# Kernel optimization log

Measured on AMD Instinct MI355X. Metric: run time of the kernel, lower is better.

The kernel has to match this reference:

```python
import jax, jax.numpy as jnp
import numpy as np

C, H, V, K, B, T = 1024, 256, 10000, 32, 8, 256
K1K = 2 * K + 1


def setup_inputs() -> dict:
    key = jax.random.key(0)
    ks = jax.random.split(key, 12)
    s = 0.05
    n = lambda k, shp: jax.random.normal(k, shp, dtype=jnp.float32) * s
    z = lambda shp: jnp.zeros(shp, dtype=jnp.float32)
    return {
        'text': jax.random.randint(ks[0], (B, T), 0, V, dtype=jnp.int32),
        'start_emb': n(ks[1], (H,)),
        'start_lin_W': n(ks[2], (H, H)), 'start_lin_b': z((H,)),
        'start_res_W1': n(ks[3], (2, H, H)), 'start_res_b1': z((2, H)),
        'start_res_W2': n(ks[4], (2, H, H)), 'start_res_b2': z((2, H)),
        'state_emb': n(ks[5], (C, H)),
        'next_state_emb': n(ks[6], (C, H)),
        'preterminal_emb': n(ks[7], (C, H)),
        'term_res_W1': n(ks[8], (2, H, H)), 'term_res_b1': z((2, H)),
        'term_res_W2': n(ks[9], (2, H, H)), 'term_res_b2': z((2, H)),
        'terminal_emb': n(ks[10], (V, H)),
        'col_banded_transition': n(ks[11], (C, K1K)),
    }


def _res(x, W1, b1, W2, b2):
    # ResLayer: x + ReLU(Linear(ReLU(Linear(x))))
    h = jax.nn.relu(x @ W1.T + b1)
    h = jax.nn.relu(h @ W2.T + b2)
    return x + h


def _band_to_dense(band):
    # BandedMatrix(band[None], K, K, fill=0).to_dense(): dense[i, i+d] = band[i, d+K] for |d|<=K
    offs = jnp.arange(-K, K + 1)                  # (K1K,)
    rows = jnp.arange(C)
    cols = rows[:, None] + offs[None, :]          # (C, K1K)
    valid = (cols >= 0) & (cols < C)
    vals = jnp.where(valid, band, 0.0)
    return jnp.zeros((C, C), band.dtype).at[rows[:, None], jnp.clip(cols, 0, C - 1)].add(vals)


def reference(text, start_emb, start_lin_W, start_lin_b,
              start_res_W1, start_res_b1, start_res_W2, start_res_b2,
              state_emb, next_state_emb, preterminal_emb,
              term_res_W1, term_res_b1, term_res_W2, term_res_b2,
              terminal_emb, col_banded_transition):
    # start(): MLP(start_emb) @ next_state_emb.T (tie_start), log_softmax -> (C,)
    fx = start_emb @ start_lin_W.T + start_lin_b
    for i in range(2):
        fx = _res(fx, start_res_W1[i], start_res_b1[i], start_res_W2[i], start_res_b2[i])
    start = jax.nn.log_softmax(fx @ next_state_emb.T)

    # transition(): dense logits + banded logits (band_method='product'), row log_softmax -> (C, C)
    logits = state_emb @ next_state_emb.T
    trans = jax.nn.log_softmax(logits + _band_to_dense(col_banded_transition), axis=-1)

    # emission(): terminal_mlp(preterminal_emb) @ terminal_emb.T, log_softmax -> (C, V)
    ft = preterminal_emb
    for i in range(2):
        ft = _res(ft, term_res_W1[i], term_res_b1[i], term_res_W2[i], term_res_b2[i])
    emit_T = jax.nn.log_softmax(ft @ terminal_emb.T, axis=-1).T  # (V, C)

    # HMM forward algorithm over time (log semiring)
    alpha = start[None, :] + emit_T[text[:, 0]]  # (B, C)

    def step(alpha, toks):
        # alpha_next[b, j] = logsumexp_i(alpha[b, i] + trans[i, j]) + emit[j, tok_b]
        a = jax.nn.logsumexp(alpha[:, :, None] + trans[None], axis=1) + emit_T[toks]
        return a, None

    alpha, _ = jax.lax.scan(step, alpha, text[:, 1:].T)
    return jax.nn.logsumexp(alpha, axis=-1)  # (B,) log-evidence
```

## Files before the change

### kernel.cpp

```cpp
#include <hip/hip_runtime.h>

constexpr int C = 1024, H = 256, V = 10000, K = 32, B = 8, T = 256, K1K = 65;
constexpr int DB = 32;
constexpr int GSCAN = B * DB;
constexpr float LV = 9.210340371976184f;
constexpr unsigned SENT = 0x80000000u;

#define DEV static __device__ __forceinline__

typedef float f4 __attribute__((ext_vector_type(4)));

DEV void gstore(float* p, float v) {
  __hip_atomic_store((unsigned*)p, __float_as_uint(v), __ATOMIC_RELAXED, __HIP_MEMORY_SCOPE_AGENT);
}
DEV float gload(const float* p) {
  return __uint_as_float(__hip_atomic_load((unsigned*)p, __ATOMIC_RELAXED, __HIP_MEMORY_SCOPE_AGENT));
}

__global__ void __launch_bounds__(256) k_pre(
    const float* __restrict__ semb, const float* __restrict__ linW, const float* __restrict__ linb,
    const float* __restrict__ srW1, const float* __restrict__ srb1,
    const float* __restrict__ srW2, const float* __restrict__ srb2,
    const float* __restrict__ nse, const float* __restrict__ se,
    const float* __restrict__ pre, const float* __restrict__ trW1, const float* __restrict__ trb1,
    const float* __restrict__ trW2, const float* __restrict__ trb2,
    const float* __restrict__ band,
    float* __restrict__ pay, float* __restrict__ startv,
    float* __restrict__ ft, float* __restrict__ PT) {
  __shared__ float smem[10504];
  const int bid = blockIdx.x, tid = threadIdx.x;

  if (bid < 16) {
    unsigned* p = (unsigned*)pay;
    #pragma unroll
    for (int k = 0; k < 8; ++k) p[bid * 2048 + k * 256 + tid] = SENT;
    return;
  }

  if (bid == 16) {
    float* sa = smem;
    float* fx = smem + 256;
    float* hh = smem + 512;
    float* sl = smem + 768;
    float* red = smem + 1792;
    sa[tid] = semb[tid];
    __syncthreads();
    float acc = linb[tid];
    for (int h = 0; h < H; ++h) acc += sa[h] * linW[tid * H + h];
    fx[tid] = acc;
    __syncthreads();
    for (int l = 0; l < 2; ++l) {
      float a1 = srb1[l * H + tid];
      const float* w1 = srW1 + (size_t)l * H * H + (size_t)tid * H;
      for (int h = 0; h < H; ++h) a1 += fx[h] * w1[h];
      hh[tid] = fmaxf(a1, 0.f);
      __syncthreads();
      float a2 = srb2[l * H + tid];
      const float* w2 = srW2 + (size_t)l * H * H + (size_t)tid * H;
      for (int h = 0; h < H; ++h) a2 += hh[h] * w2[h];
      __syncthreads();
      fx[tid] += fmaxf(a2, 0.f);
      __syncthreads();
    }
    for (int q = 0; q < 4; ++q) {
      int c = q * 256 + tid;
      const float* nr = nse + (size_t)c * H;
      float s = 0.f;
      for (int h = 0; h < H; ++h) s += fx[h] * nr[h];
      sl[c] = s;
    }
    __syncthreads();
    float s = 0.f;
    for (int q = 0; q < 4; ++q) s += __expf(sl[q * 256 + tid]);
    red[tid] = s; __syncthreads();
    for (int off = 128; off > 0; off >>= 1) { if (tid < off) red[tid] += red[tid + off]; __syncthreads(); }
    float lse = __logf(red[0]);
    for (int q = 0; q < 4; ++q) { int c = q * 256 + tid; startv[c] = sl[c] - lse; }
    return;
  }

  if (bid < 81) {
    float* x = smem;
    float* hh = smem + 4096;
    int r0 = (bid - 17) * 16;
    for (int r = 0; r < 16; ++r) x[r * 256 + tid] = pre[(size_t)(r0 + r) * H + tid];
    __syncthreads();
    for (int l = 0; l < 2; ++l) {
      {
        const f4* w = (const f4*)(trW1 + (size_t)l * H * H + (size_t)tid * H);
        float a[16];
        #pragma unroll
        for (int r = 0; r < 16; ++r) a[r] = 0.f;
        for (int h4 = 0; h4 < H / 4; ++h4) {
          f4 wv = w[h4];
          #pragma unroll
          for (int r = 0; r < 16; ++r) {
            f4 xv = *(const f4*)&x[r * 256 + h4 * 4];
            a[r] += wv.x * xv.x + wv.y * xv.y + wv.z * xv.z + wv.w * xv.w;
          }
        }
        float bb = trb1[l * H + tid];
        #pragma unroll
        for (int r = 0; r < 16; ++r) hh[r * 256 + tid] = fmaxf(a[r] + bb, 0.f);
      }
      __syncthreads();
      {
        const f4* w = (const f4*)(trW2 + (size_t)l * H * H + (size_t)tid * H);
        float a[16];
        #pragma unroll
        for (int r = 0; r < 16; ++r) a[r] = 0.f;
        for (int h4 = 0; h4 < H / 4; ++h4) {
          f4 wv = w[h4];
          #pragma unroll
          for (int r = 0; r < 16; ++r) {
            f4 xv = *(const f4*)&hh[r * 256 + h4 * 4];
            a[r] += wv.x * xv.x + wv.y * xv.y + wv.z * xv.z + wv.w * xv.w;
          }
        }
        float bb = trb2[l * H + tid];
        #pragma unroll
        for (int r = 0; r < 16; ++r) x[r * 256 + tid] += fmaxf(a[r] + bb, 0.f);
      }
      __syncthreads();
    }
    for (int r = 0; r < 16; ++r) ft[(size_t)(r0 + r) * H + tid] = x[r * 256 + tid];
    return;
  }

  {
    float* sv = smem;
    float* sl = smem + 2048;
    float* pr = smem + 10240;
    float* iv = smem + 10496;
    int i0 = (bid - 81) * 8;
    for (int r = 0; r < 8; ++r) sv[r * 256 + tid] = se[(size_t)(i0 + r) * H + tid];
    __syncthreads();
    for (int jq = 0; jq < 4; ++jq) {
      int j = jq * 256 + tid;
      const f4* nr = (const f4*)(nse + (size_t)j * H);
      float a[8];
      #pragma unroll
      for (int r = 0; r < 8; ++r) a[r] = 0.f;
      for (int h4 = 0; h4 < H / 4; ++h4) {
        f4 nv = nr[h4];
        #pragma unroll
        for (int r = 0; r < 8; ++r) {
          f4 s4 = *(const f4*)&sv[r * 256 + h4 * 4];
          a[r] += nv.x * s4.x + nv.y * s4.y + nv.z * s4.z + nv.w * s4.w;
        }
      }
      #pragma unroll
      for (int r = 0; r < 8; ++r) sl[r * 1024 + j] = a[r];
    }
    __syncthreads();
    if (tid < K1K) {
      #pragma unroll
      for (int r = 0; r < 8; ++r) {
        int col = i0 + r + tid - K;
        if (col >= 0 && col < C) sl[r * 1024 + col] += band[(size_t)(i0 + r) * K1K + tid];
      }
    }
    __syncthreads();
    {
      int row = tid >> 5, lane32 = tid & 31;
      float s = 0.f;
      for (int k = 0; k < 32; ++k) {
        int idx = row * 1024 + lane32 + k * 32;
        float e = __expf(sl[idx]);
        sl[idx] = e;
        s += e;
      }
      pr[tid] = s;
    }
    __syncthreads();
    if (tid < 8) {
      float s = 0.f;
      for (int k = 0; k < 32; ++k) s += pr[tid * 32 + k];
      iv[tid] = 1.f / s;
    }
    __syncthreads();
    for (int jq = 0; jq < 4; ++jq) {
      int j = jq * 256 + tid;
      f4 o0, o1;
      o0.x = sl[0 * 1024 + j] * iv[0]; o0.y = sl[1 * 1024 + j] * iv[1];
      o0.z = sl[2 * 1024 + j] * iv[2]; o0.w = sl[3 * 1024 + j] * iv[3];
      o1.x = sl[4 * 1024 + j] * iv[4]; o1.y = sl[5 * 1024 + j] * iv[5];
      o1.z = sl[6 * 1024 + j] * iv[6]; o1.w = sl[7 * 1024 + j] * iv[7];
      f4* dst = (f4*)(PT + (size_t)j * C + i0);
      dst[0] = o0; dst[1] = o1;
    }
  }
}

__global__ void __launch_bounds__(256) k_denom_part(
    const float* __restrict__ ft, const float* __restrict__ term, float* __restrict__ dpart) {
  constexpr int TJ = 16, VC = V / 8;
  __shared__ float shs[TJ * 4];
  int tid = threadIdx.x, lane = tid & 63, w = tid >> 6;
  int jg = blockIdx.x >> 3, vc = blockIdx.x & 7;
  const f4* fb = (const f4*)(ft + (size_t)jg * TJ * H);
  float rs[TJ];
  #pragma unroll
  for (int r = 0; r < TJ; ++r) rs[r] = 0.f;
  int v0 = vc * VC;
  {
    const f4* t0 = (const f4*)(term + (size_t)(v0 + tid) * H);
    const f4* t1 = t0 + 256 * (H / 4);
    const f4* t2 = t1 + 256 * (H / 4);
    const f4* t3 = t2 + 256 * (H / 4);
    float a0[TJ], a1[TJ], a2[TJ], a3[TJ];
    #pragma unroll
    for (int r = 0; r < TJ; ++r) { a0[r] = 0.f; a1[r] = 0.f; a2[r] = 0.f; a3[r] = 0.f; }
    for (int h4 = 0; h4 < H / 4; ++h4) {
      f4 w0 = t0[h4], w1 = t1[h4], w2 = t2[h4], w3 = t3[h4];
      #pragma unroll
      for (int r = 0; r < TJ; ++r) {
        f4 f = fb[r * (H / 4) + h4];
        a0[r] += f.x * w0.x + f.y * w0.y + f.z * w0.z + f.w * w0.w;
        a1[r] += f.x * w1.x + f.y * w1.y + f.z * w1.z + f.w * w1.w;
        a2[r] += f.x * w2.x + f.y * w2.y + f.z * w2.z + f.w * w2.w;
        a3[r] += f.x * w3.x + f.y * w3.y + f.z * w3.z + f.w * w3.w;
      }
    }
    #pragma unroll
    for (int r = 0; r < TJ; ++r)
      rs[r] += __expf(a0[r]) + __expf(a1[r]) + __expf(a2[r]) + __expf(a3[r]);
  }
  if (tid < VC - 1024) {
    const f4* tt = (const f4*)(term + (size_t)(v0 + 1024 + tid) * H);
    float at[TJ];
    #pragma unroll
    for (int r = 0; r < TJ; ++r) at[r] = 0.f;
    for (int h4 = 0; h4 < H / 4; ++h4) {
      f4 wt = tt[h4];
      #pragma unroll
      for (int r = 0; r < TJ; ++r) {
        f4 f = fb[r * (H / 4) + h4];
        at[r] += f.x * wt.x + f.y * wt.y + f.z * wt.z + f.w * wt.w;
      }
    }
    #pragma unroll
    for (int r = 0; r < TJ; ++r) rs[r] += __expf(at[r]);
  }
  #pragma unroll
  for (int r = 0; r < TJ; ++r) {
    float s = rs[r];
    #pragma unroll
    for (int off = 32; off > 0; off >>= 1) s += __shfl_xor(s, off);
    if (lane == 0) shs[r * 4 + w] = s;
  }
  __syncthreads();
  if (tid < TJ) {
    float s = shs[tid * 4] + shs[tid * 4 + 1] + shs[tid * 4 + 2] + shs[tid * 4 + 3];
    dpart[(jg * TJ + tid) * 8 + vc] = s;
  }
}

__global__ void __launch_bounds__(256) k_eemit(
    const int* __restrict__ text, const float* __restrict__ ft,
    const float* __restrict__ dpart, const float* __restrict__ term,
    float* __restrict__ eem) {
  __shared__ float tk[32 * 256];
  __shared__ int ids[32];
  const int tid = threadIdx.x, bid = blockIdx.x;
  const int n0 = (bid >> 1) * 32, jh = bid & 1;
  if (tid < 32) {
    int n = n0 + tid;
    ids[tid] = text[(n & 7) * T + (n >> 3)];
  }
  __syncthreads();
  for (int r = 0; r < 32; ++r) tk[r * 256 + tid] = term[(size_t)ids[r] * H + tid];
  __syncthreads();
  for (int q = 0; q < 2; ++q) {
    int j = jh * 512 + q * 256 + tid;
    const f4* fr = (const f4*)(ft + (size_t)j * H);
    float acc[32];
    #pragma unroll
    for (int r = 0; r < 32; ++r) acc[r] = 0.f;
    for (int h4 = 0; h4 < H / 4; ++h4) {
      f4 fv = fr[h4];
      #pragma unroll
      for (int r = 0; r < 32; ++r) {
        f4 tv = *(const f4*)&tk[r * 256 + h4 * 4];
        acc[r] += fv.x * tv.x + fv.y * tv.y + fv.z * tv.z + fv.w * tv.w;
      }
    }
    f4 d0 = *(const f4*)&dpart[j * 8];
    f4 d1 = *(const f4*)&dpart[j * 8 + 4];
    float dj = __logf(d0.x + d0.y + d0.z + d0.w + d1.x + d1.y + d1.z + d1.w);
    #pragma unroll
    for (int r = 0; r < 32; ++r)
      eem[(size_t)(n0 + r) * C + j] = __expf(acc[r] - dj + LV);
  }
}

#define PLOADA(k, ofs) \
  asm volatile("global_load_dwordx4 %0, %1, off offset:" #ofs : "=v"(p##k) : "v"(pb));
#define PDOT(k) { f4 x = *(const f4*)&us[ubo + (k) * 4]; facc += p##k * x; }

__global__ void __launch_bounds__(256, 1) k_scan(
    const float* __restrict__ PT, const float* __restrict__ eem,
    const float* __restrict__ startv, float* __restrict__ pay,
    float* __restrict__ umax, float* __restrict__ out) {
  __shared__ __align__(16) float us[8 * 132];
  __shared__ __align__(16) float wv[32];
  __shared__ float fred[256];
  const int tid = threadIdx.x, bid = blockIdx.x;
  const int b = bid & 7, blk = bid >> 3;
  const int jloc = tid >> 3, s = tid & 7;
  const int myj = blk * 32 + jloc;
  const bool owner = (s == 0);

  const float* pb = PT + (size_t)myj * C + s * 128;
  f4 p0, p1, p2, p3, p4, p5, p6, p7, p8, p9, p10, p11, p12, p13, p14, p15;
  f4 p16, p17, p18, p19, p20, p21, p22, p23, p24, p25, p26, p27, p28, p29, p30, p31;
  PLOADA(0, 0)    PLOADA(1, 16)   PLOADA(2, 32)   PLOADA(3, 48)
  PLOADA(4, 64)   PLOADA(5, 80)   PLOADA(6, 96)   PLOADA(7, 112)
  PLOADA(8, 128)  PLOADA(9, 144)  PLOADA(10, 160) PLOADA(11, 176)
  PLOADA(12, 192) PLOADA(13, 208) PLOADA(14, 224) PLOADA(15, 240)
  PLOADA(16, 256) PLOADA(17, 272) PLOADA(18, 288) PLOADA(19, 304)
  PLOADA(20, 320) PLOADA(21, 336) PLOADA(22, 352) PLOADA(23, 368)
  PLOADA(24, 384) PLOADA(25, 400) PLOADA(26, 416) PLOADA(27, 432)
  PLOADA(28, 448) PLOADA(29, 464) PLOADA(30, 480) PLOADA(31, 496)

  float Sacc = 0.f;

  if (owner) {
    float u0 = __expf(startv[myj]) * eem[(size_t)b * C + myj];
    gstore(&pay[(size_t)b * C + myj], u0);
  }
  float em = owner ? eem[((size_t)B + b) * C + myj] : 0.f;

  const int pi = tid * 4;
  const int ph = (pi >> 7) * 132 + (pi & 127);
  const int ubo = s * 132;

  for (int t = 1; t < T; ++t) {
    {
      const float* src = pay + (size_t)((t - 1) & 3) * (B * C) + (size_t)b * C + pi;
      f4 r;
      for (;;) {
        asm volatile("global_load_dwordx4 %0, %1, off sc0 sc1\n\ts_waitcnt vmcnt(0)"
                     : "=v"(r) : "v"(src) : "memory");
        unsigned bits = __float_as_uint(r.x) | __float_as_uint(r.y) |
                        __float_as_uint(r.z) | __float_as_uint(r.w);
        if (!(bits & 0x80000000u)) break;
        __builtin_amdgcn_s_sleep(1);
      }
      *(f4*)&us[ph] = r;
    }
    __syncthreads();

    float em_next = em;
    if (owner && t + 1 < T) em_next = eem[((size_t)(t + 1) * B + b) * C + myj];

    float imt = 1.f;
    if (owner && (t & 7) == 1 && t > 1) {
      float m = gload(&umax[((t - 1) >> 3) * 8 + b]);
      imt = 1.f / m;
      Sacc += __logf(m);
    }

    f4 facc = {0.f, 0.f, 0.f, 0.f};
    PDOT(0) PDOT(1) PDOT(2) PDOT(3) PDOT(4) PDOT(5) PDOT(6) PDOT(7)
    PDOT(8) PDOT(9) PDOT(10) PDOT(11) PDOT(12) PDOT(13) PDOT(14) PDOT(15)
    PDOT(16) PDOT(17) PDOT(18) PDOT(19) PDOT(20) PDOT(21) PDOT(22) PDOT(23)
    PDOT(24) PDOT(25) PDOT(26) PDOT(27) PDOT(28) PDOT(29) PDOT(30) PDOT(31)
    float acc = facc.x + facc.y + facc.z + facc.w;
    acc += __shfl_xor(acc, 1);
    acc += __shfl_xor(acc, 2);
    acc += __shfl_xor(acc, 4);

    if (owner) wv[jloc] = acc * imt * em;
    __syncthreads();

    if (blk == 0 && (t & 7) == 0) {
      if (tid == 0) {
        float m = wv[0];
        #pragma unroll
        for (int j2 = 1; j2 < 32; ++j2) m = fmaxf(m, wv[j2]);
        gstore(&umax[(t >> 3) * 8 + b], m);
        asm volatile("s_waitcnt vmcnt(0)" ::: "memory");
      }
      __syncthreads();
    }

    if (tid < 8) {
      f4 pv4 = *(const f4*)&wv[tid * 4];
      float* dst = pay + (size_t)(t & 3) * (B * C) + (size_t)b * C + blk * 32 + tid * 4;
      asm volatile("global_store_dwordx4 %0, %1, off sc0 sc1" :: "v"(dst), "v"(pv4) : "memory");
    }

    if (tid < 8) {
      float* dst = pay + (size_t)((t + 2) & 3) * (B * C) + (size_t)b * C + blk * 32 + tid * 4;
      f4 sn;
      sn.x = sn.y = sn.z = sn.w = __uint_as_float(SENT);
      asm volatile("global_store_dwordx4 %0, %1, off sc0 sc1" :: "v"(dst), "v"(sn) : "memory");
    }
    em = em_next;
  }

  if (blk == 0) {
    {
      const float* src = pay + (size_t)((T - 1) & 3) * (B * C) + (size_t)b * C + pi;
      f4 r;
      for (;;) {
        asm volatile("global_load_dwordx4 %0, %1, off sc0 sc1\n\ts_waitcnt vmcnt(0)"
                     : "=v"(r) : "v"(src) : "memory");
        unsigned bits = __float_as_uint(r.x) | __float_as_uint(r.y) |
                        __float_as_uint(r.z) | __float_as_uint(r.w);
        if (!(bits & 0x80000000u)) break;
        __builtin_amdgcn_s_sleep(1);
      }
      fred[tid] = r.x + r.y + r.z + r.w;
    }
    __syncthreads();
    for (int off = 128; off > 0; off >>= 1) {
      if (tid < off) fred[tid] += fred[tid + off];
      __syncthreads();
    }
    if (tid == 0) out[b] = -(float)T * LV + Sacc + __logf(fred[0]);
  }
}

extern "C" void kernel_launch(void* const* d_in, const int* in_sizes, int n_in,
                              void* d_out, int out_size, void* d_ws, size_t ws_size,
                              hipStream_t stream) {
  const int*   text  = (const int*)  d_in[0];
  const float* semb  = (const float*)d_in[1];
  const float* slinW = (const float*)d_in[2];
  const float* slinb = (const float*)d_in[3];
  const float* srW1  = (const float*)d_in[4];
  const float* srb1  = (const float*)d_in[5];
  const float* srW2  = (const float*)d_in[6];
  const float* srb2  = (const float*)d_in[7];
  const float* stemb = (const float*)d_in[8];
  const float* nse   = (const float*)d_in[9];
  const float* pre   = (const float*)d_in[10];
  const float* trW1  = (const float*)d_in[11];
  const float* trb1  = (const float*)d_in[12];
  const float* trW2  = (const float*)d_in[13];
  const float* trb2  = (const float*)d_in[14];
  const float* term  = (const float*)d_in[15];
  const float* band  = (const float*)d_in[16];

  float* ws     = (float*)d_ws;
  float* PT     = ws;
  float* eem    = PT + (size_t)C * C;
  float* pay    = eem + (size_t)T * B * C;
  float* ftb    = pay + 4 * B * C;
  float* startv = ftb + (size_t)C * H;
  float* dpart  = startv + C;
  float* umax   = dpart + C * 8;

  k_pre<<<209, 256, 0, stream>>>(semb, slinW, slinb, srW1, srb1, srW2, srb2,
                                 nse, stemb, pre, trW1, trb1, trW2, trb2, band,
                                 pay, startv, ftb, PT);
  k_denom_part<<<(C / 16) * 8, 256, 0, stream>>>(ftb, term, dpart);
  k_eemit<<<128, 256, 0, stream>>>(text, ftb, dpart, term, eem);
  k_scan<<<GSCAN, 256, 0, stream>>>(PT, eem, startv, pay, umax, (float*)d_out);
}
```

Baseline: 861.9 us.

## Process four batch rows per scan workgroup to halve scan grid size

Each scan workgroup now serially handles four batch elements instead of one, so the grid shrinks from 256 to 64 workgroups and the register-resident transition slice is reused across four batches. Per time step each block runs four sequential poll/dot/store phases. This cuts the number of cross-workgroup participants per step but serializes batch work inside a workgroup, lengthening the critical path of each time step.

```diff
diff --git a/kernel.cpp b/kernel.cpp
--- a/kernel.cpp
+++ b/kernel.cpp
@@ -2,7 +2,8 @@
 
 constexpr int C = 1024, H = 256, V = 10000, K = 32, B = 8, T = 256, K1K = 65;
 constexpr int DB = 32;
-constexpr int GSCAN = B * DB;
+constexpr int NB = 4;
+constexpr int GSCAN = (B / NB) * DB;
 constexpr float LV = 9.210340371976184f;
 constexpr unsigned SENT = 0x80000000u;
 
@@ -306,7 +307,8 @@
   __shared__ __align__(16) float wv[32];
   __shared__ float fred[256];
   const int tid = threadIdx.x, bid = blockIdx.x;
-  const int b = bid & 7, blk = bid >> 3;
+  const int g = bid & 1, blk = bid >> 1;
+  const int b0 = g * NB;
   const int jloc = tid >> 3, s = tid & 7;
   const int myj = blk * 32 + jloc;
   const bool owner = (s == 0);
@@ -323,103 +325,119 @@
   PLOADA(24, 384) PLOADA(25, 400) PLOADA(26, 416) PLOADA(27, 432)
   PLOADA(28, 448) PLOADA(29, 464) PLOADA(30, 480) PLOADA(31, 496)
 
-  float Sacc = 0.f;
+  float Sacc[NB];
+  float em[NB];
+  #pragma unroll
+  for (int k = 0; k < NB; ++k) Sacc[k] = 0.f;
 
   if (owner) {
-    float u0 = __expf(startv[myj]) * eem[(size_t)b * C + myj];
-    gstore(&pay[(size_t)b * C + myj], u0);
-  }
-  float em = owner ? eem[((size_t)B + b) * C + myj] : 0.f;
+    float sv0 = __expf(startv[myj]);
+    #pragma unroll
+    for (int k = 0; k < NB; ++k)
+      gstore(&pay[(size_t)(b0 + k) * C + myj], sv0 * eem[(size_t)(b0 + k) * C + myj]);
+  }
+  #pragma unroll
+  for (int k = 0; k < NB; ++k)
+    em[k] = owner ? eem[((size_t)B + (b0 + k)) * C + myj] : 0.f;
 
   const int pi = tid * 4;
   const int ph = (pi >> 7) * 132 + (pi & 127);
   const int ubo = s * 132;
 
   for (int t = 1; t < T; ++t) {
-    {
-      const float* src = pay + (size_t)((t - 1) & 3) * (B * C) + (size_t)b * C + pi;
-      f4 r;
-      for (;;) {
-        asm volatile("global_load_dwordx4 %0, %1, off sc0 sc1\n\ts_waitcnt vmcnt(0)"
-                     : "=v"(r) : "v"(src) : "memory");
-        unsigned bits = __float_as_uint(r.x) | __float_as_uint(r.y) |
-                        __float_as_uint(r.z) | __float_as_uint(r.w);
-        if (!(bits & 0x80000000u)) break;
-        __builtin_amdgcn_s_sleep(1);
-      }
-      *(f4*)&us[ph] = r;
-    }
-    __syncthreads();
-
-    float em_next = em;
-    if (owner && t + 1 < T) em_next = eem[((size_t)(t + 1) * B + b) * C + myj];
-
-    float imt = 1.f;
-    if (owner && (t & 7) == 1 && t > 1) {
-      float m = gload(&umax[((t - 1) >> 3) * 8 + b]);
-      imt = 1.f / m;
-      Sacc += __logf(m);
-    }
-
-    f4 facc = {0.f, 0.f, 0.f, 0.f};
-    PDOT(0) PDOT(1) PDOT(2) PDOT(3) PDOT(4) PDOT(5) PDOT(6) PDOT(7)
-    PDOT(8) PDOT(9) PDOT(10) PDOT(11) PDOT(12) PDOT(13) PDOT(14) PDOT(15)
-    PDOT(16) PDOT(17) PDOT(18) PDOT(19) PDOT(20) PDOT(21) PDOT(22) PDOT(23)
-    PDOT(24) PDOT(25) PDOT(26) PDOT(27) PDOT(28) PDOT(29) PDOT(30) PDOT(31)
-    float acc = facc.x + facc.y + facc.z + facc.w;
-    acc += __shfl_xor(acc, 1);
-    acc += __shfl_xor(acc, 2);
-    acc += __shfl_xor(acc, 4);
-
-    if (owner) wv[jloc] = acc * imt * em;
-    __syncthreads();
-
-    if (blk == 0 && (t & 7) == 0) {
-      if (tid == 0) {
-        float m = wv[0];
-        #pragma unroll
-        for (int j2 = 1; j2 < 32; ++j2) m = fmaxf(m, wv[j2]);
-        gstore(&umax[(t >> 3) * 8 + b], m);
-        asm volatile("s_waitcnt vmcnt(0)" ::: "memory");
-      }
-      __syncthreads();
-    }
-
-    if (tid < 8) {
-      f4 pv4 = *(const f4*)&wv[tid * 4];
-      float* dst = pay + (size_t)(t & 3) * (B * C) + (size_t)b * C + blk * 32 + tid * 4;
-      asm volatile("global_store_dwordx4 %0, %1, off sc0 sc1" :: "v"(dst), "v"(pv4) : "memory");
-    }
-
-    if (tid < 8) {
-      float* dst = pay + (size_t)((t + 2) & 3) * (B * C) + (size_t)b * C + blk * 32 + tid * 4;
-      f4 sn;
-      sn.x = sn.y = sn.z = sn.w = __uint_as_float(SENT);
-      asm volatile("global_store_dwordx4 %0, %1, off sc0 sc1" :: "v"(dst), "v"(sn) : "memory");
-    }
-    em = em_next;
+    #pragma unroll
+    for (int k = 0; k < NB; ++k) {
+      const int b = b0 + k;
+      {
+        const float* src = pay + (size_t)((t - 1) & 3) * (B * C) + (size_t)b * C + pi;
+        f4 r;
+        for (;;) {
+          asm volatile("global_load_dwordx4 %0, %1, off sc0 sc1\n\ts_waitcnt vmcnt(0)"
+                       : "=v"(r) : "v"(src) : "memory");
+          unsigned bits = __float_as_uint(r.x) | __float_as_uint(r.y) |
+                          __float_as_uint(r.z) | __float_as_uint(r.w);
+          if (!(bits & 0x80000000u)) break;
+          __builtin_amdgcn_s_sleep(1);
+        }
+        *(f4*)&us[ph] = r;
+      }
+      __syncthreads();
+
+      float em_next = em[k];
+      if (owner && t + 1 < T) em_next = eem[((size_t)(t + 1) * B + b) * C + myj];
+
+      float imt = 1.f;
+      if (owner && (t & 7) == 1 && t > 1) {
+        float m = gload(&umax[((t - 1) >> 3) * 8 + b]);
+        imt = 1.f / m;
+        Sacc[k] += __logf(m);
+      }
+
+      f4 facc = {0.f, 0.f, 0.f, 0.f};
+      PDOT(0) PDOT(1) PDOT(2) PDOT(3) PDOT(4) PDOT(5) PDOT(6) PDOT(7)
+      PDOT(8) PDOT(9) PDOT(10) PDOT(11) PDOT(12) PDOT(13) PDOT(14) PDOT(15)
+      PDOT(16) PDOT(17) PDOT(18) PDOT(19) PDOT(20) PDOT(21) PDOT(22) PDOT(23)
+      PDOT(24) PDOT(25) PDOT(26) PDOT(27) PDOT(28) PDOT(29) PDOT(30) PDOT(31)
+      float acc = facc.x + facc.y + facc.z + facc.w;
+      acc += __shfl_xor(acc, 1);
+      acc += __shfl_xor(acc, 2);
+      acc += __shfl_xor(acc, 4);
+
+      if (owner) wv[jloc] = acc * imt * em[k];
+      __syncthreads();
+
+      if (blk == 0 && (t & 7) == 0) {
+        if (tid == 0) {
+          float m = wv[0];
+          #pragma unroll
+          for (int j2 = 1; j2 < 32; ++j2) m = fmaxf(m, wv[j2]);
+          gstore(&umax[(t >> 3) * 8 + b], m);
+          asm volatile("s_waitcnt vmcnt(0)" ::: "memory");
+        }
+        __syncthreads();
+      }
+
+      if (tid < 8) {
+        f4 pv4 = *(const f4*)&wv[tid * 4];
+        float* dst = pay + (size_t)(t & 3) * (B * C) + (size_t)b * C + blk * 32 + tid * 4;
+        asm volatile("global_store_dwordx4 %0, %1, off sc0 sc1" :: "v"(dst), "v"(pv4) : "memory");
+      }
+
+      if (tid < 8) {
+        float* dst = pay + (size_t)((t + 2) & 3) * (B * C) + (size_t)b * C + blk * 32 + tid * 4;
+        f4 sn;
+        sn.x = sn.y = sn.z = sn.w = __uint_as_float(SENT);
+        asm volatile("global_store_dwordx4 %0, %1, off sc0 sc1" :: "v"(dst), "v"(sn) : "memory");
+      }
+      em[k] = em_next;
+    }
   }
 
   if (blk == 0) {
-    {
-      const float* src = pay + (size_t)((T - 1) & 3) * (B * C) + (size_t)b * C + pi;
-      f4 r;
-      for (;;) {
-        asm volatile("global_load_dwordx4 %0, %1, off sc0 sc1\n\ts_waitcnt vmcnt(0)"
-                     : "=v"(r) : "v"(src) : "memory");
-        unsigned bits = __float_as_uint(r.x) | __float_as_uint(r.y) |
-                        __float_as_uint(r.z) | __float_as_uint(r.w);
-        if (!(bits & 0x80000000u)) break;
-        __builtin_amdgcn_s_sleep(1);
-      }
-      fred[tid] = r.x + r.y + r.z + r.w;
-    }
-    __syncthreads();
-    for (int off = 128; off > 0; off >>= 1) {
-      if (tid < off) fred[tid] += fred[tid + off];
-      __syncthreads();
-    }
-    if (tid == 0) out[b] = -(float)T * LV + Sacc + __logf(fred[0]);
+    #pragma unroll
+    for (int kk = 0; kk < NB; ++kk) {
+      const int b = b0 + kk;
+      {
+        const float* src = pay + (size_t)((T - 1) & 3) * (B * C) + (size_t)b * C + pi;
+        f4 r;
+        for (;;) {
+          asm volatile("global_load_dwordx4 %0, %1, off sc0 sc1\n\ts_waitcnt vmcnt(0)"
+                       : "=v"(r) : "v"(src) : "memory");
+          unsigned bits = __float_as_uint(r.x) | __float_as_uint(r.y) |
+                          __float_as_uint(r.z) | __float_as_uint(r.w);
+          if (!(bits & 0x80000000u)) break;
+          __builtin_amdgcn_s_sleep(1);
+        }
+        fred[tid] = r.x + r.y + r.z + r.w;
+      }
+      __syncthreads();
+      for (int off = 128; off > 0; off >>= 1) {
+        if (tid < off) fred[tid] += fred[tid + off];
+        __syncthreads();
+      }
+      if (tid == 0) out[b] = -(float)T * LV + Sacc[kk] + __logf(fred[0]);
+      __syncthreads();
+    }
   }
 }
 
```

After: 1.754 ms. 2.03x slower.

## Stage preterminal features in LDS and double rows per block in denom kernel

Applied to the files above, without the earlier changes.

The emission-denominator kernel now copies a 32-row tile of terminal-MLP features into padded shared memory and reads it from there, instead of reading 16 rows straight from global memory. Each block covers twice as many rows, so half as many blocks are launched and each terminal-embedding row is loaded from global memory half as often. The inner loop now keeps one accumulator set of 32 per pass over five 256-vocab chunks, replacing four interleaved 16-row sets. This lowers register pressure but gives less ILP per terminal load, and the smaller grid (256 blocks) may leave compute units underused.

```diff
diff --git a/kernel.cpp b/kernel.cpp
--- a/kernel.cpp
+++ b/kernel.cpp
@@ -194,53 +194,34 @@
 
 __global__ void __launch_bounds__(256) k_denom_part(
     const float* __restrict__ ft, const float* __restrict__ term, float* __restrict__ dpart) {
-  constexpr int TJ = 16, VC = V / 8;
+  constexpr int TJ = 32, VC = V / 8;
+  constexpr int RS = 264;
+  __shared__ float ftL[TJ * RS];
   __shared__ float shs[TJ * 4];
   int tid = threadIdx.x, lane = tid & 63, w = tid >> 6;
   int jg = blockIdx.x >> 3, vc = blockIdx.x & 7;
-  const f4* fb = (const f4*)(ft + (size_t)jg * TJ * H);
+  for (int r = 0; r < TJ; ++r) ftL[r * RS + tid] = ft[(size_t)(jg * TJ + r) * H + tid];
+  __syncthreads();
   float rs[TJ];
   #pragma unroll
   for (int r = 0; r < TJ; ++r) rs[r] = 0.f;
   int v0 = vc * VC;
-  {
-    const f4* t0 = (const f4*)(term + (size_t)(v0 + tid) * H);
-    const f4* t1 = t0 + 256 * (H / 4);
-    const f4* t2 = t1 + 256 * (H / 4);
-    const f4* t3 = t2 + 256 * (H / 4);
-    float a0[TJ], a1[TJ], a2[TJ], a3[TJ];
-    #pragma unroll
-    for (int r = 0; r < TJ; ++r) { a0[r] = 0.f; a1[r] = 0.f; a2[r] = 0.f; a3[r] = 0.f; }
+  for (int vstep = 0; vstep < 5; ++vstep) {
+    if (vstep == 4 && tid >= VC - 1024) break;
+    const f4* tr = (const f4*)(term + (size_t)(v0 + vstep * 256 + tid) * H);
+    float acc[TJ];
+    #pragma unroll
+    for (int r = 0; r < TJ; ++r) acc[r] = 0.f;
     for (int h4 = 0; h4 < H / 4; ++h4) {
-      f4 w0 = t0[h4], w1 = t1[h4], w2 = t2[h4], w3 = t3[h4];
+      f4 tv = tr[h4];
       #pragma unroll
       for (int r = 0; r < TJ; ++r) {
-        f4 f = fb[r * (H / 4) + h4];
-        a0[r] += f.x * w0.x + f.y * w0.y + f.z * w0.z + f.w * w0.w;
-        a1[r] += f.x * w1.x + f.y * w1.y + f.z * w1.z + f.w * w1.w;
-        a2[r] += f.x * w2.x + f.y * w2.y + f.z * w2.z + f.w * w2.w;
-        a3[r] += f.x * w3.x + f.y * w3.y + f.z * w3.z + f.w * w3.w;
-      }
-    }
-    #pragma unroll
-    for (int r = 0; r < TJ; ++r)
-      rs[r] += __expf(a0[r]) + __expf(a1[r]) + __expf(a2[r]) + __expf(a3[r]);
-  }
-  if (tid < VC - 1024) {
-    const f4* tt = (const f4*)(term + (size_t)(v0 + 1024 + tid) * H);
-    float at[TJ];
-    #pragma unroll
-    for (int r = 0; r < TJ; ++r) at[r] = 0.f;
-    for (int h4 = 0; h4 < H / 4; ++h4) {
-      f4 wt = tt[h4];
-      #pragma unroll
-      for (int r = 0; r < TJ; ++r) {
-        f4 f = fb[r * (H / 4) + h4];
-        at[r] += f.x * wt.x + f.y * wt.y + f.z * wt.z + f.w * wt.w;
-      }
-    }
-    #pragma unroll
-    for (int r = 0; r < TJ; ++r) rs[r] += __expf(at[r]);
+        f4 f = *(const f4*)&ftL[r * RS + h4 * 4];
+        acc[r] += tv.x * f.x + tv.y * f.y + tv.z * f.z + tv.w * f.w;
+      }
+    }
+    #pragma unroll
+    for (int r = 0; r < TJ; ++r) rs[r] += __expf(acc[r]);
   }
   #pragma unroll
   for (int r = 0; r < TJ; ++r) {
@@ -456,7 +437,7 @@
   k_pre<<<209, 256, 0, stream>>>(semb, slinW, slinb, srW1, srb1, srW2, srb2,
                                  nse, stemb, pre, trW1, trb1, trW2, trb2, band,
                                  pay, startv, ftb, PT);
-  k_denom_part<<<(C / 16) * 8, 256, 0, stream>>>(ftb, term, dpart);
+  k_denom_part<<<(C / 32) * 8, 256, 0, stream>>>(ftb, term, dpart);
   k_eemit<<<128, 256, 0, stream>>>(text, ftb, dpart, term, eem);
   k_scan<<<GSCAN, 256, 0, stream>>>(PT, eem, startv, pay, umax, (float*)d_out);
 }
```

After: 994.8 us. 15.4% more time.
